# Performance work log

Measured on AMD Instinct MI355X. Metric: run time of the kernel, lower is better.

## Reference

```python
import jax, jax.numpy as jnp
import numpy as np

N = 20000
IN_C = 512
HID = 64
H1 = 8
OUT_C = 256
E = 320000
NEG_SLOPE = 0.2


def gat_conv(x, src, dst, W, a_src, a_dst, b, concat):
    # PyG GATConv (shared lin for src/dst), inference mode (no dropout).
    H, C = a_src.shape
    h = (x @ W).reshape(N, H, C)                      # [N,H,C]
    alpha_src = (h * a_src[None]).sum(-1)             # [N,H]
    alpha_dst = (h * a_dst[None]).sum(-1)             # [N,H]
    alpha = jax.nn.leaky_relu(alpha_src[src] + alpha_dst[dst], NEG_SLOPE)  # [E,H]
    # segment softmax over incoming edges of each dst node
    amax = jax.ops.segment_max(alpha, dst, num_segments=N)
    amax = jnp.where(jnp.isfinite(amax), amax, 0.0)
    ex = jnp.exp(alpha - amax[dst])
    denom = jax.ops.segment_sum(ex, dst, num_segments=N)
    coef = ex / (denom[dst] + 1e-16)                  # [E,H]
    msg = h[src] * coef[:, :, None]                   # [E,H,C]
    out = jax.ops.segment_sum(msg, dst, num_segments=N)  # [N,H,C]
    out = out.reshape(N, H * C) if concat else out.mean(axis=1)
    return out + b


def setup_inputs() -> dict:
    key = jax.random.key(0)
    ks = jax.random.split(key, 10)
    x = jax.random.normal(ks[0], (N, IN_C), dtype=jnp.float32)
    edge_index = jax.random.randint(ks[1], (2, E), 0, N, dtype=jnp.int32)
    s1 = 1.0 / np.sqrt(IN_C)
    s2 = 1.0 / np.sqrt(HID * H1)
    W1 = jax.random.uniform(ks[2], (IN_C, H1 * HID), jnp.float32, -s1, s1)
    att_src1 = jax.random.uniform(ks[3], (H1, HID), jnp.float32, -s1, s1)
    att_dst1 = jax.random.uniform(ks[4], (H1, HID), jnp.float32, -s1, s1)
    b1 = jnp.zeros((H1 * HID,), jnp.float32)
    W2 = jax.random.uniform(ks[5], (H1 * HID, OUT_C), jnp.float32, -s2, s2)
    att_src2 = jax.random.uniform(ks[6], (1, OUT_C), jnp.float32, -s2, s2)
    att_dst2 = jax.random.uniform(ks[7], (1, OUT_C), jnp.float32, -s2, s2)
    b2 = jnp.zeros((OUT_C,), jnp.float32)
    return {"x": x, "edge_index": edge_index, "W1": W1, "att_src1": att_src1,
            "att_dst1": att_dst1, "b1": b1, "W2": W2, "att_src2": att_src2,
            "att_dst2": att_dst2, "b2": b2}


def reference(x, edge_index, W1, att_src1, att_dst1, b1, W2, att_src2, att_dst2, b2):
    # add self-loops (PyG GATConv default add_self_loops=True)
    loop = jnp.arange(N, dtype=edge_index.dtype)
    src = jnp.concatenate([edge_index[0], loop])
    dst = jnp.concatenate([edge_index[1], loop])
    h = gat_conv(x, src, dst, W1, att_src1, att_dst1, b1, concat=True)
    h = jax.nn.elu(h)
    out = gat_conv(h, src, dst, W2, att_src2, att_dst2, b2, concat=False)
    return jax.nn.log_softmax(out, axis=1)
```

## Files before the change

### kernel.cpp

```cpp
#include <hip/hip_runtime.h>
#include <math.h>

#define N_NODES 20000
#define IN_CH   512
#define HID_TOT 512
#define OUT_CH  256
#define N_EDGE  320000
#define TOT_EDGE (N_EDGE + N_NODES)

typedef __attribute__((ext_vector_type(8))) short short8;
typedef __attribute__((ext_vector_type(4))) float f32x4;
typedef __attribute__((ext_vector_type(2))) float f32x2;

__device__ __forceinline__ ushort f2bf(float f) {
    union { float f; unsigned u; } v; v.f = f;
    unsigned u = v.u;
    return (ushort)((u + 0x7fffu + ((u >> 16) & 1u)) >> 16);
}

__device__ __forceinline__ void glds16(const ushort* g, ushort* l) {
    __builtin_amdgcn_global_load_lds(
        (const __attribute__((address_space(1))) void*)g,
        (__attribute__((address_space(3))) void*)l, 16, 0, 0);
}

__device__ __forceinline__ float lrelu(float a) { return fmaxf(a, 0.2f * a); }

#define NA_BLK (N_NODES * IN_CH / 4 / 256)
#define NB_BLK ((IN_CH / 64) * (HID_TOT / 4))
#define NC_BLK ((HID_TOT / 64) * (OUT_CH / 4))
#define NZ_BLK ((N_NODES + 255) / 256)
__global__ __launch_bounds__(256) void prep_kernel(const float* __restrict__ x,
                                                   ushort* __restrict__ xb,
                                                   const float* __restrict__ W1,
                                                   ushort* __restrict__ w1t,
                                                   const float* __restrict__ W2,
                                                   ushort* __restrict__ w2t,
                                                   int* __restrict__ counts,
                                                   float* __restrict__ as2,
                                                   float* __restrict__ ad2) {
    int b = blockIdx.x;
    int t = threadIdx.x;
    if (b < NA_BLK) {
        int i = b * 256 + t;
        float4 v = *(const float4*)&x[(size_t)i * 4];
        ushort4 o = make_ushort4(f2bf(v.x), f2bf(v.y), f2bf(v.z), f2bf(v.w));
        *(ushort4*)&xb[(size_t)i * 4] = o;
    } else if (b < NA_BLK + NB_BLK) {
        int bb = b - NA_BLK;
        int k = (bb & 7) * 64 + (t & 63);
        int n = (bb >> 3) * 4 + (t >> 6);
        w1t[(size_t)n * IN_CH + k] = f2bf(W1[(size_t)k * HID_TOT + n]);
    } else if (b < NA_BLK + NB_BLK + NC_BLK) {
        int bb = b - NA_BLK - NB_BLK;
        int k = (bb & 7) * 64 + (t & 63);
        int n = (bb >> 3) * 4 + (t >> 6);
        w2t[(size_t)n * HID_TOT + k] = f2bf(W2[(size_t)k * OUT_CH + n]);
    } else {
        int i = (b - NA_BLK - NB_BLK - NC_BLK) * 256 + t;
        if (i < N_NODES) { counts[i] = 0; as2[i] = 0.f; ad2[i] = 0.f; }
    }
}

__global__ void hist_kernel(const int* __restrict__ ei, int* __restrict__ counts) {
    int e = blockIdx.x * blockDim.x + threadIdx.x;
    if (e >= TOT_EDGE) return;
    int d = (e < N_EDGE) ? ei[N_EDGE + e] : (e - N_EDGE);
    atomicAdd(&counts[d], 1);
}

__global__ __launch_bounds__(1024) void scan_kernel(const int* __restrict__ counts,
                                                    int* __restrict__ offsets,
                                                    int* __restrict__ cursors) {
    const int C = (N_NODES + 1023) / 1024;
    int t = threadIdx.x;
    int lane = t & 63, wid = t >> 6;
    int base = t * C;
    int sum = 0;
#pragma unroll
    for (int i = 0; i < C; i++) {
        int idx = base + i;
        if (idx < N_NODES) sum += counts[idx];
    }
    int val = sum;
#pragma unroll
    for (int off = 1; off < 64; off <<= 1) {
        int y = __shfl_up(val, off);
        if (lane >= off) val += y;
    }
    __shared__ int wsum[16], woff[16], stotal;
    if (lane == 63) wsum[wid] = val;
    __syncthreads();
    if (t == 0) {
        int r = 0;
        for (int w = 0; w < 16; w++) { woff[w] = r; r += wsum[w]; }
        stotal = r;
    }
    __syncthreads();
    int running = woff[wid] + (val - sum);
#pragma unroll
    for (int i = 0; i < C; i++) {
        int idx = base + i;
        if (idx < N_NODES) {
            offsets[idx] = running;
            cursors[idx] = running;
            running += counts[idx];
        }
    }
    if (t == 0) offsets[N_NODES] = stotal;
}

__global__ void scatter_kernel(const int* __restrict__ ei, int* __restrict__ cursors,
                               int* __restrict__ srcs) {
    int e = blockIdx.x * blockDim.x + threadIdx.x;
    if (e >= TOT_EDGE) return;
    int s, d;
    if (e < N_EDGE) { s = ei[e]; d = ei[N_EDGE + e]; } else { s = e - N_EDGE; d = s; }
    int pos = atomicAdd(&cursors[d], 1);
    srcs[pos] = s;
}

__global__ __launch_bounds__(256) void gemm_mfma_kernel(const ushort* __restrict__ A,
                                                        const ushort* __restrict__ Bt,
                                                        unsigned char* __restrict__ Cf8,
                                                        const float* __restrict__ asrc,
                                                        const float* __restrict__ adst,
                                                        float* __restrict__ as_out,
                                                        float* __restrict__ ad_out,
                                                        int M, int N, int K, int layer1) {
    __shared__ ushort As[128 * 64];
    __shared__ ushort Bs[64 * 64];
    int t = threadIdx.x;
    int lane = t & 63;
    int wave = t >> 6;
    int wm = wave * 32;
    int bm = blockIdx.y * 128, bn = blockIdx.x * 64;
    int q = lane >> 4, l15 = lane & 15;

    const ushort* Aptr[4]; ushort* Alds[4];
    const ushort* Bptr[2]; ushort* Blds[2];
#pragma unroll
    for (int k = 0; k < 4; k++) {
        int c = t + 256 * k;
        int r = c >> 3, kqs = c & 7;
        int kqg = kqs ^ (r & 7);
        int ar = bm + r; if (ar >= M) ar = M - 1;
        Aptr[k] = A + (size_t)ar * K + kqg * 8;
        Alds[k] = &As[c * 8];
    }
#pragma unroll
    for (int k = 0; k < 2; k++) {
        int c = t + 256 * k;
        int r = c >> 3, kqs = c & 7;
        int kqg = kqs ^ (r & 7);
        Bptr[k] = Bt + (size_t)(bn + r) * K + kqg * 8;
        Blds[k] = &Bs[c * 8];
    }

    f32x4 acc[2][4];
#pragma unroll
    for (int i = 0; i < 2; i++)
#pragma unroll
        for (int j = 0; j < 4; j++) acc[i][j] = f32x4{0.f, 0.f, 0.f, 0.f};

    for (int k0 = 0; k0 < K; k0 += 64) {
        __syncthreads();
        glds16(Aptr[0] + k0, Alds[0]);
        glds16(Aptr[1] + k0, Alds[1]);
        glds16(Aptr[2] + k0, Alds[2]);
        glds16(Aptr[3] + k0, Alds[3]);
        glds16(Bptr[0] + k0, Blds[0]);
        glds16(Bptr[1] + k0, Blds[1]);
        __syncthreads();

#pragma unroll
        for (int s = 0; s < 2; s++) {
            int kq = s * 4 + q;
            short8 af[2], bf[4];
#pragma unroll
            for (int i = 0; i < 2; i++) {
                int row = wm + i * 16 + l15;
                int slot = kq ^ (row & 7);
                af[i] = *(const short8*)&As[row * 64 + slot * 8];
            }
#pragma unroll
            for (int j = 0; j < 4; j++) {
                int row = j * 16 + l15;
                int slot = kq ^ (row & 7);
                bf[j] = *(const short8*)&Bs[row * 64 + slot * 8];
            }
#pragma unroll
            for (int i = 0; i < 2; i++)
#pragma unroll
                for (int j = 0; j < 4; j++)
                    acc[i][j] = __builtin_amdgcn_mfma_f32_16x16x32_bf16(af[i], bf[j], acc[i][j], 0, 0, 0);
        }
    }

    float av[4], dv[4];
#pragma unroll
    for (int j = 0; j < 4; j++) {
        int cg = bn + j * 16 + l15;
        av[j] = asrc[cg];
        dv[j] = adst[cg];
    }
    float ps[2][4], pd[2][4];
#pragma unroll
    for (int i = 0; i < 2; i++)
#pragma unroll
        for (int r = 0; r < 4; r++) {
            float p = 0.f, d = 0.f;
#pragma unroll
            for (int j = 0; j < 4; j++) {
                p = fmaf(acc[i][j][r], av[j], p);
                d = fmaf(acc[i][j][r], dv[j], d);
            }
            ps[i][r] = p; pd[i][r] = d;
        }
#pragma unroll
    for (int off = 1; off < 16; off <<= 1) {
#pragma unroll
        for (int i = 0; i < 2; i++)
#pragma unroll
            for (int r = 0; r < 4; r++) {
                ps[i][r] += __shfl_xor(ps[i][r], off);
                pd[i][r] += __shfl_xor(pd[i][r], off);
            }
    }

    int hidx = blockIdx.x;
#pragma unroll
    for (int i = 0; i < 2; i++) {
#pragma unroll
        for (int r = 0; r < 4; r++) {
            int rg = bm + wm + i * 16 + q * 4 + r;
            if (rg < M) {
#pragma unroll
                for (int j = 0; j < 4; j++) {
                    int cg = bn + j * 16 + l15;
                    int w8 = __builtin_amdgcn_cvt_pk_fp8_f32(acc[i][j][r], acc[i][j][r], 0, false);
                    Cf8[(size_t)rg * N + cg] = (unsigned char)(w8 & 0xff);
                }
                if (l15 == 0) {
                    if (layer1) {
                        as_out[rg * 8 + hidx] = ps[i][r];
                        ad_out[rg * 8 + hidx] = pd[i][r];
                    } else {
                        atomicAdd(&as_out[rg], ps[i][r]);
                        atomicAdd(&ad_out[rg], pd[i][r]);
                    }
                }
            }
        }
    }
}

__global__ __launch_bounds__(64) void agg1_kernel(const unsigned char* __restrict__ h1f,
                                                  const float* __restrict__ as1,
                                                  const float* __restrict__ ad1,
                                                  const int* __restrict__ offsets,
                                                  const int* __restrict__ srcs,
                                                  const float* __restrict__ b1,
                                                  ushort* __restrict__ h1ab) {
    int v = blockIdx.x;
    int t = threadIdx.x;
    int h = t >> 3;
    int c8 = t << 3;
    int s = offsets[v], e = offsets[v + 1];
    float adv = ad1[v * 8 + h];

    float denom = 0.f;
    float acc[8];
#pragma unroll
    for (int k = 0; k < 8; k++) acc[k] = 0.f;

    int i = s;
    for (; i + 8 <= e; i += 8) {
        int sn[8];
#pragma unroll
        for (int j = 0; j < 8; j++) sn[j] = srcs[i + j];
        uint2 r[8];
#pragma unroll
        for (int j = 0; j < 8; j++)
            r[j] = *(const uint2*)&h1f[(size_t)sn[j] * HID_TOT + c8];
        float w[8];
#pragma unroll
        for (int j = 0; j < 8; j++) {
            float a = lrelu(as1[sn[j] * 8 + h] + adv);
            w[j] = __expf(a);
            denom += w[j];
        }
#pragma unroll
        for (int j = 0; j < 8; j++) {
            f32x2 pa = __builtin_amdgcn_cvt_pk_f32_fp8(r[j].x, false);
            f32x2 pb = __builtin_amdgcn_cvt_pk_f32_fp8(r[j].x, true);
            f32x2 pc = __builtin_amdgcn_cvt_pk_f32_fp8(r[j].y, false);
            f32x2 pdd = __builtin_amdgcn_cvt_pk_f32_fp8(r[j].y, true);
            acc[0] = fmaf(w[j], pa.x, acc[0]); acc[1] = fmaf(w[j], pa.y, acc[1]);
            acc[2] = fmaf(w[j], pb.x, acc[2]); acc[3] = fmaf(w[j], pb.y, acc[3]);
            acc[4] = fmaf(w[j], pc.x, acc[4]); acc[5] = fmaf(w[j], pc.y, acc[5]);
            acc[6] = fmaf(w[j], pdd.x, acc[6]); acc[7] = fmaf(w[j], pdd.y, acc[7]);
        }
    }
    for (; i + 4 <= e; i += 4) {
        int sn[4];
#pragma unroll
        for (int j = 0; j < 4; j++) sn[j] = srcs[i + j];
        uint2 r[4];
#pragma unroll
        for (int j = 0; j < 4; j++)
            r[j] = *(const uint2*)&h1f[(size_t)sn[j] * HID_TOT + c8];
#pragma unroll
        for (int j = 0; j < 4; j++) {
            float a = lrelu(as1[sn[j] * 8 + h] + adv);
            float w = __expf(a);
            denom += w;
            f32x2 pa = __builtin_amdgcn_cvt_pk_f32_fp8(r[j].x, false);
            f32x2 pb = __builtin_amdgcn_cvt_pk_f32_fp8(r[j].x, true);
            f32x2 pc = __builtin_amdgcn_cvt_pk_f32_fp8(r[j].y, false);
            f32x2 pdd = __builtin_amdgcn_cvt_pk_f32_fp8(r[j].y, true);
            acc[0] = fmaf(w, pa.x, acc[0]); acc[1] = fmaf(w, pa.y, acc[1]);
            acc[2] = fmaf(w, pb.x, acc[2]); acc[3] = fmaf(w, pb.y, acc[3]);
            acc[4] = fmaf(w, pc.x, acc[4]); acc[5] = fmaf(w, pc.y, acc[5]);
            acc[6] = fmaf(w, pdd.x, acc[6]); acc[7] = fmaf(w, pdd.y, acc[7]);
        }
    }
    for (; i < e; i++) {
        int sn = srcs[i];
        uint2 r = *(const uint2*)&h1f[(size_t)sn * HID_TOT + c8];
        float a = lrelu(as1[sn * 8 + h] + adv);
        float w = __expf(a);
        denom += w;
        f32x2 pa = __builtin_amdgcn_cvt_pk_f32_fp8(r.x, false);
        f32x2 pb = __builtin_amdgcn_cvt_pk_f32_fp8(r.x, true);
        f32x2 pc = __builtin_amdgcn_cvt_pk_f32_fp8(r.y, false);
        f32x2 pdd = __builtin_amdgcn_cvt_pk_f32_fp8(r.y, true);
        acc[0] = fmaf(w, pa.x, acc[0]); acc[1] = fmaf(w, pa.y, acc[1]);
        acc[2] = fmaf(w, pb.x, acc[2]); acc[3] = fmaf(w, pb.y, acc[3]);
        acc[4] = fmaf(w, pc.x, acc[4]); acc[5] = fmaf(w, pc.y, acc[5]);
        acc[6] = fmaf(w, pdd.x, acc[6]); acc[7] = fmaf(w, pdd.y, acc[7]);
    }

    float inv = 1.f / (denom + 1e-16f);
    short8 ov;
#pragma unroll
    for (int k = 0; k < 8; k++) {
        float o = acc[k] * inv + b1[c8 + k];
        o = (o > 0.f) ? o : expm1f(o);
        ov[k] = (short)f2bf(o);
    }
    *(short8*)&h1ab[(size_t)v * HID_TOT + c8] = ov;
}

__global__ __launch_bounds__(64) void agg2_kernel(const unsigned char* __restrict__ h2f,
                                                  const float* __restrict__ as2,
                                                  const float* __restrict__ ad2,
                                                  const int* __restrict__ offsets,
                                                  const int* __restrict__ srcs,
                                                  const float* __restrict__ b2,
                                                  float* __restrict__ out) {
    int v = blockIdx.x;
    int t = threadIdx.x;
    int c4 = t << 2;
    int s = offsets[v], e = offsets[v + 1];
    float adv = ad2[v];

    float denom = 0.f;
    float acc[4];
#pragma unroll
    for (int k = 0; k < 4; k++) acc[k] = 0.f;

    int i = s;
    for (; i + 8 <= e; i += 8) {
        int sn[8];
#pragma unroll
        for (int j = 0; j < 8; j++) sn[j] = srcs[i + j];
        unsigned u[8];
#pragma unroll
        for (int j = 0; j < 8; j++)
            u[j] = *(const unsigned*)&h2f[(size_t)sn[j] * OUT_CH + c4];
        float w[8];
#pragma unroll
        for (int j = 0; j < 8; j++) {
            float a = lrelu(as2[sn[j]] + adv);
            w[j] = __expf(a);
            denom += w[j];
        }
#pragma unroll
        for (int j = 0; j < 8; j++) {
            f32x2 pa = __builtin_amdgcn_cvt_pk_f32_fp8(u[j], false);
            f32x2 pb = __builtin_amdgcn_cvt_pk_f32_fp8(u[j], true);
            acc[0] = fmaf(w[j], pa.x, acc[0]); acc[1] = fmaf(w[j], pa.y, acc[1]);
            acc[2] = fmaf(w[j], pb.x, acc[2]); acc[3] = fmaf(w[j], pb.y, acc[3]);
        }
    }
    for (; i + 4 <= e; i += 4) {
        int sn[4];
#pragma unroll
        for (int j = 0; j < 4; j++) sn[j] = srcs[i + j];
        unsigned u[4];
#pragma unroll
        for (int j = 0; j < 4; j++)
            u[j] = *(const unsigned*)&h2f[(size_t)sn[j] * OUT_CH + c4];
#pragma unroll
        for (int j = 0; j < 4; j++) {
            float a = lrelu(as2[sn[j]] + adv);
            float w = __expf(a);
            denom += w;
            f32x2 pa = __builtin_amdgcn_cvt_pk_f32_fp8(u[j], false);
            f32x2 pb = __builtin_amdgcn_cvt_pk_f32_fp8(u[j], true);
            acc[0] = fmaf(w, pa.x, acc[0]); acc[1] = fmaf(w, pa.y, acc[1]);
            acc[2] = fmaf(w, pb.x, acc[2]); acc[3] = fmaf(w, pb.y, acc[3]);
        }
    }
    for (; i < e; i++) {
        int sn = srcs[i];
        unsigned u = *(const unsigned*)&h2f[(size_t)sn * OUT_CH + c4];
        float a = lrelu(as2[sn] + adv);
        float w = __expf(a);
        denom += w;
        f32x2 pa = __builtin_amdgcn_cvt_pk_f32_fp8(u, false);
        f32x2 pb = __builtin_amdgcn_cvt_pk_f32_fp8(u, true);
        acc[0] = fmaf(w, pa.x, acc[0]); acc[1] = fmaf(w, pa.y, acc[1]);
        acc[2] = fmaf(w, pb.x, acc[2]); acc[3] = fmaf(w, pb.y, acc[3]);
    }

    float inv = 1.f / (denom + 1e-16f);
    float4 bb = *(const float4*)&b2[c4];
    float4 x;
    x.x = acc[0] * inv + bb.x; x.y = acc[1] * inv + bb.y;
    x.z = acc[2] * inv + bb.z; x.w = acc[3] * inv + bb.w;

    float mm = fmaxf(fmaxf(x.x, x.y), fmaxf(x.z, x.w));
#pragma unroll
    for (int off = 1; off < 64; off <<= 1) mm = fmaxf(mm, __shfl_xor(mm, off));
    float sum = __expf(x.x - mm) + __expf(x.y - mm) + __expf(x.z - mm) + __expf(x.w - mm);
#pragma unroll
    for (int off = 1; off < 64; off <<= 1) sum += __shfl_xor(sum, off);
    float ls = logf(sum);
    float4 o;
    o.x = x.x - mm - ls; o.y = x.y - mm - ls; o.z = x.z - mm - ls; o.w = x.w - mm - ls;
    *(float4*)&out[(size_t)v * OUT_CH + c4] = o;
}

static inline size_t align256(size_t x) { return (x + 255) & ~(size_t)255; }

extern "C" void kernel_launch(void* const* d_in, const int* in_sizes, int n_in,
                              void* d_out, int out_size, void* d_ws, size_t ws_size,
                              hipStream_t stream) {
    const float* x    = (const float*)d_in[0];
    const int*   ei   = (const int*)d_in[1];
    const float* W1   = (const float*)d_in[2];
    const float* as1w = (const float*)d_in[3];
    const float* ad1w = (const float*)d_in[4];
    const float* b1   = (const float*)d_in[5];
    const float* W2   = (const float*)d_in[6];
    const float* as2w = (const float*)d_in[7];
    const float* ad2w = (const float*)d_in[8];
    const float* b2   = (const float*)d_in[9];
    float* out = (float*)d_out;

    char* p = (char*)d_ws;
    unsigned char* h1f = (unsigned char*)p; p += align256((size_t)N_NODES * HID_TOT);
    unsigned char* h2f = (unsigned char*)p; p += align256((size_t)N_NODES * OUT_CH);
    ushort* xb   = (ushort*)p; p += align256(sizeof(ushort) * (size_t)N_NODES * IN_CH);
    ushort* h1ab = xb;
    ushort* w1t  = (ushort*)p; p += align256(sizeof(ushort) * (size_t)IN_CH * HID_TOT);
    ushort* w2t  = (ushort*)p; p += align256(sizeof(ushort) * (size_t)HID_TOT * OUT_CH);
    float* as1  = (float*)p; p += align256(sizeof(float) * (size_t)N_NODES * 8);
    float* ad1  = (float*)p; p += align256(sizeof(float) * (size_t)N_NODES * 8);
    float* as2  = (float*)p; p += align256(sizeof(float) * (size_t)N_NODES);
    float* ad2  = (float*)p; p += align256(sizeof(float) * (size_t)N_NODES);
    int* counts  = (int*)p; p += align256(sizeof(int) * (size_t)N_NODES);
    int* offsets = (int*)p; p += align256(sizeof(int) * (size_t)(N_NODES + 1));
    int* cursors = (int*)p; p += align256(sizeof(int) * (size_t)N_NODES);
    int* srcs    = (int*)p; p += align256(sizeof(int) * (size_t)TOT_EDGE);

    prep_kernel<<<NA_BLK + NB_BLK + NC_BLK + NZ_BLK, 256, 0, stream>>>(
        x, xb, W1, w1t, W2, w2t, counts, as2, ad2);

    int eb = (TOT_EDGE + 255) / 256;
    hist_kernel<<<eb, 256, 0, stream>>>(ei, counts);
    scan_kernel<<<1, 1024, 0, stream>>>(counts, offsets, cursors);
    scatter_kernel<<<eb, 256, 0, stream>>>(ei, cursors, srcs);

    gemm_mfma_kernel<<<dim3(HID_TOT / 64, (N_NODES + 127) / 128), 256, 0, stream>>>(
        xb, w1t, h1f, as1w, ad1w, as1, ad1, N_NODES, HID_TOT, IN_CH, 1);
    agg1_kernel<<<N_NODES, 64, 0, stream>>>(h1f, as1, ad1, offsets, srcs, b1, h1ab);

    gemm_mfma_kernel<<<dim3(OUT_CH / 64, (N_NODES + 127) / 128), 256, 0, stream>>>(
        h1ab, w2t, h2f, as2w, ad2w, as2, ad2, N_NODES, OUT_CH, HID_TOT, 0);
    agg2_kernel<<<N_NODES, 64, 0, stream>>>(h2f, as2, ad2, offsets, srcs, b2, out);
}
```

Measured before the change: 276.8 us.

## Enlarge GEMM tile to 128x128 and pack four nodes per aggregation block

The GEMM tile grows from 128x64 to 128x128, with waves arranged 2x2 so each computes a 64x64 sub-tile and per-head attention indices are derived from the column half. This raises register-level reuse of A and B fragments but halves the grid, leaving fewer blocks for 20000x256 and 20000x512 outputs. The aggregation kernels now run four destination nodes per 256-thread block instead of one node per 64-thread block, which cuts the block count and scheduling overhead. A risk is reduced occupancy or tail imbalance because the larger GEMM needs more accumulator registers.

Result: no change. 276.5 us (-0.1%).

```diff
diff --git a/kernel.cpp b/kernel.cpp
--- a/kernel.cpp
+++ b/kernel.cpp
@@ -120,25 +120,26 @@
     srcs[pos] = s;
 }
 
-__global__ __launch_bounds__(256) void gemm_mfma_kernel(const ushort* __restrict__ A,
-                                                        const ushort* __restrict__ Bt,
-                                                        unsigned char* __restrict__ Cf8,
-                                                        const float* __restrict__ asrc,
-                                                        const float* __restrict__ adst,
-                                                        float* __restrict__ as_out,
-                                                        float* __restrict__ ad_out,
-                                                        int M, int N, int K, int layer1) {
+__global__ __launch_bounds__(256, 2) void gemm_mfma_kernel(const ushort* __restrict__ A,
+                                                           const ushort* __restrict__ Bt,
+                                                           unsigned char* __restrict__ Cf8,
+                                                           const float* __restrict__ asrc,
+                                                           const float* __restrict__ adst,
+                                                           float* __restrict__ as_out,
+                                                           float* __restrict__ ad_out,
+                                                           int M, int N, int K, int layer1) {
     __shared__ ushort As[128 * 64];
-    __shared__ ushort Bs[64 * 64];
+    __shared__ ushort Bs[128 * 64];
     int t = threadIdx.x;
     int lane = t & 63;
     int wave = t >> 6;
-    int wm = wave * 32;
-    int bm = blockIdx.y * 128, bn = blockIdx.x * 64;
+    int wr = (wave >> 1) * 64;
+    int wc = (wave & 1) * 64;
+    int bm = blockIdx.y * 128, bn = blockIdx.x * 128;
     int q = lane >> 4, l15 = lane & 15;
 
     const ushort* Aptr[4]; ushort* Alds[4];
-    const ushort* Bptr[2]; ushort* Blds[2];
+    const ushort* Bptr[4]; ushort* Blds[4];
 #pragma unroll
     for (int k = 0; k < 4; k++) {
         int c = t + 256 * k;
@@ -147,19 +148,13 @@
         int ar = bm + r; if (ar >= M) ar = M - 1;
         Aptr[k] = A + (size_t)ar * K + kqg * 8;
         Alds[k] = &As[c * 8];
-    }
-#pragma unroll
-    for (int k = 0; k < 2; k++) {
-        int c = t + 256 * k;
-        int r = c >> 3, kqs = c & 7;
-        int kqg = kqs ^ (r & 7);
         Bptr[k] = Bt + (size_t)(bn + r) * K + kqg * 8;
         Blds[k] = &Bs[c * 8];
     }
 
-    f32x4 acc[2][4];
-#pragma unroll
-    for (int i = 0; i < 2; i++)
+    f32x4 acc[4][4];
+#pragma unroll
+    for (int i = 0; i < 4; i++)
 #pragma unroll
         for (int j = 0; j < 4; j++) acc[i][j] = f32x4{0.f, 0.f, 0.f, 0.f};
 
@@ -171,26 +166,28 @@
         glds16(Aptr[3] + k0, Alds[3]);
         glds16(Bptr[0] + k0, Blds[0]);
         glds16(Bptr[1] + k0, Blds[1]);
+        glds16(Bptr[2] + k0, Blds[2]);
+        glds16(Bptr[3] + k0, Blds[3]);
         __syncthreads();
 
 #pragma unroll
         for (int s = 0; s < 2; s++) {
             int kq = s * 4 + q;
-            short8 af[2], bf[4];
-#pragma unroll
-            for (int i = 0; i < 2; i++) {
-                int row = wm + i * 16 + l15;
+            short8 af[4], bf[4];
+#pragma unroll
+            for (int i = 0; i < 4; i++) {
+                int row = wr + i * 16 + l15;
                 int slot = kq ^ (row & 7);
                 af[i] = *(const short8*)&As[row * 64 + slot * 8];
             }
 #pragma unroll
             for (int j = 0; j < 4; j++) {
-                int row = j * 16 + l15;
+                int row = wc + j * 16 + l15;
                 int slot = kq ^ (row & 7);
                 bf[j] = *(const short8*)&Bs[row * 64 + slot * 8];
             }
 #pragma unroll
-            for (int i = 0; i < 2; i++)
+            for (int i = 0; i < 4; i++)
 #pragma unroll
                 for (int j = 0; j < 4; j++)
                     acc[i][j] = __builtin_amdgcn_mfma_f32_16x16x32_bf16(af[i], bf[j], acc[i][j], 0, 0, 0);
@@ -200,13 +197,13 @@
     float av[4], dv[4];
 #pragma unroll
     for (int j = 0; j < 4; j++) {
-        int cg = bn + j * 16 + l15;
+        int cg = bn + wc + j * 16 + l15;
         av[j] = asrc[cg];
         dv[j] = adst[cg];
     }
-    float ps[2][4], pd[2][4];
-#pragma unroll
-    for (int i = 0; i < 2; i++)
+    float ps[4][4], pd[4][4];
+#pragma unroll
+    for (int i = 0; i < 4; i++)
 #pragma unroll
         for (int r = 0; r < 4; r++) {
             float p = 0.f, d = 0.f;
@@ -220,7 +217,7 @@
 #pragma unroll
     for (int off = 1; off < 16; off <<= 1) {
 #pragma unroll
-        for (int i = 0; i < 2; i++)
+        for (int i = 0; i < 4; i++)
 #pragma unroll
             for (int r = 0; r < 4; r++) {
                 ps[i][r] += __shfl_xor(ps[i][r], off);
@@ -228,16 +225,16 @@
             }
     }
 
-    int hidx = blockIdx.x;
-#pragma unroll
-    for (int i = 0; i < 2; i++) {
+    int hidx = blockIdx.x * 2 + (wave & 1);
+#pragma unroll
+    for (int i = 0; i < 4; i++) {
 #pragma unroll
         for (int r = 0; r < 4; r++) {
-            int rg = bm + wm + i * 16 + q * 4 + r;
+            int rg = bm + wr + i * 16 + q * 4 + r;
             if (rg < M) {
 #pragma unroll
                 for (int j = 0; j < 4; j++) {
-                    int cg = bn + j * 16 + l15;
+                    int cg = bn + wc + j * 16 + l15;
                     int w8 = __builtin_amdgcn_cvt_pk_fp8_f32(acc[i][j][r], acc[i][j][r], 0, false);
                     Cf8[(size_t)rg * N + cg] = (unsigned char)(w8 & 0xff);
                 }
@@ -255,17 +252,17 @@
     }
 }
 
-__global__ __launch_bounds__(64) void agg1_kernel(const unsigned char* __restrict__ h1f,
-                                                  const float* __restrict__ as1,
-                                                  const float* __restrict__ ad1,
-                                                  const int* __restrict__ offsets,
-                                                  const int* __restrict__ srcs,
-                                                  const float* __restrict__ b1,
-                                                  ushort* __restrict__ h1ab) {
-    int v = blockIdx.x;
-    int t = threadIdx.x;
-    int h = t >> 3;
-    int c8 = t << 3;
+__global__ __launch_bounds__(256) void agg1_kernel(const unsigned char* __restrict__ h1f,
+                                                   const float* __restrict__ as1,
+                                                   const float* __restrict__ ad1,
+                                                   const int* __restrict__ offsets,
+                                                   const int* __restrict__ srcs,
+                                                   const float* __restrict__ b1,
+                                                   ushort* __restrict__ h1ab) {
+    int v = blockIdx.x * 4 + (threadIdx.x >> 6);
+    int lane = threadIdx.x & 63;
+    int h = lane >> 3;
+    int c8 = lane << 3;
     int s = offsets[v], e = offsets[v + 1];
     float adv = ad1[v * 8 + h];
 
@@ -352,16 +349,16 @@
     *(short8*)&h1ab[(size_t)v * HID_TOT + c8] = ov;
 }
 
-__global__ __launch_bounds__(64) void agg2_kernel(const unsigned char* __restrict__ h2f,
-                                                  const float* __restrict__ as2,
-                                                  const float* __restrict__ ad2,
-                                                  const int* __restrict__ offsets,
-                                                  const int* __restrict__ srcs,
-                                                  const float* __restrict__ b2,
-                                                  float* __restrict__ out) {
-    int v = blockIdx.x;
-    int t = threadIdx.x;
-    int c4 = t << 2;
+__global__ __launch_bounds__(256) void agg2_kernel(const unsigned char* __restrict__ h2f,
+                                                   const float* __restrict__ as2,
+                                                   const float* __restrict__ ad2,
+                                                   const int* __restrict__ offsets,
+                                                   const int* __restrict__ srcs,
+                                                   const float* __restrict__ b2,
+                                                   float* __restrict__ out) {
+    int v = blockIdx.x * 4 + (threadIdx.x >> 6);
+    int lane = threadIdx.x & 63;
+    int c4 = lane << 2;
     int s = offsets[v], e = offsets[v + 1];
     float adv = ad2[v];
 
@@ -484,11 +481,11 @@
     scan_kernel<<<1, 1024, 0, stream>>>(counts, offsets, cursors);
     scatter_kernel<<<eb, 256, 0, stream>>>(ei, cursors, srcs);
 
-    gemm_mfma_kernel<<<dim3(HID_TOT / 64, (N_NODES + 127) / 128), 256, 0, stream>>>(
+    gemm_mfma_kernel<<<dim3(HID_TOT / 128, (N_NODES + 127) / 128), 256, 0, stream>>>(
         xb, w1t, h1f, as1w, ad1w, as1, ad1, N_NODES, HID_TOT, IN_CH, 1);
-    agg1_kernel<<<N_NODES, 64, 0, stream>>>(h1f, as1, ad1, offsets, srcs, b1, h1ab);
-
-    gemm_mfma_kernel<<<dim3(OUT_CH / 64, (N_NODES + 127) / 128), 256, 0, stream>>>(
+    agg1_kernel<<<(N_NODES + 3) / 4, 256, 0, stream>>>(h1f, as1, ad1, offsets, srcs, b1, h1ab);
+
+    gemm_mfma_kernel<<<dim3(OUT_CH / 128, (N_NODES + 127) / 128), 256, 0, stream>>>(
         h1ab, w2t, h2f, as2w, ad2w, as2, ad2, N_NODES, OUT_CH, HID_TOT, 0);
-    agg2_kernel<<<N_NODES, 64, 0, stream>>>(h2f, as2, ad2, offsets, srcs, b2, out);
-}
+    agg2_kernel<<<(N_NODES + 3) / 4, 256, 0, stream>>>(h2f, as2, ad2, offsets, srcs, b2, out);
+}
```
